# Kernel tuning notes

Measured on AMD Instinct MI355X. Metric: run time of the kernel, lower is better.

## Reference

```python
import jax, jax.numpy as jnp
import numpy as np

B, N, M = 32, 512, 512
EPS = 0.05        # Sinkhorn entropic regularization (approximates exact EMD flow)
N_ITERS = 50      # fixed Sinkhorn iterations
NEG = -1e9        # log(0) surrogate for masked particles


def setup_inputs() -> dict:
    key = jax.random.key(0)
    k1, k2, k3, k4, k5, k6 = jax.random.split(key, 6)
    a_mask = (jax.random.uniform(k1, (B, N)) > 0.1).astype(jnp.float32)
    b_mask = (jax.random.uniform(k2, (B, M)) > 0.1).astype(jnp.float32)
    a_mask = a_mask.at[:, 0].set(1.0)  # guarantee nonempty clouds
    b_mask = b_mask.at[:, 0].set(1.0)
    pc_a = jnp.concatenate([jax.random.normal(k3, (B, N, 2)),
                            jax.random.uniform(k5, (B, N, 1), minval=0.1, maxval=1.0)], axis=-1)
    pc_b = jnp.concatenate([jax.random.normal(k4, (B, M, 2)),
                            jax.random.uniform(k6, (B, M, 1), minval=0.1, maxval=1.0)], axis=-1)
    return {"a_mask": a_mask, "pc_a": pc_a, "b_mask": b_mask, "pc_b": pc_b}


def _sinkhorn_logflow(loga, logb, logK):
    # log-domain Sinkhorn: find P with row sums exp(loga), col sums exp(logb)
    def body(i, carry):
        logu, logv = carry
        logu = loga - jax.scipy.special.logsumexp(logK + logv[:, None, :], axis=2)
        logv = logb - jax.scipy.special.logsumexp(logK + logu[:, :, None], axis=1)
        return (logu, logv)
    logu = jnp.zeros_like(loga)
    logv = jnp.zeros_like(logb)
    logu, logv = jax.lax.fori_loop(0, N_ITERS, body, (logu, logv))
    return logu[:, :, None] + logK + logv[:, None, :]  # [B, N, M]


def _emd_flow(a_pt, b_pt, dist, va, vb):
    # normalized pt distributions (emd(..., norm=True))
    aw = a_pt / jnp.sum(a_pt, axis=-1, keepdims=True)
    bw = b_pt / jnp.sum(b_pt, axis=-1, keepdims=True)
    loga = jnp.where(va, jnp.log(jnp.where(va, aw, 1.0)), NEG)
    logb = jnp.where(vb, jnp.log(jnp.where(vb, bw, 1.0)), NEG)
    logK = -dist / EPS
    flow = jnp.exp(_sinkhorn_logflow(loga, logb, logK))
    return flow * va[:, :, None].astype(flow.dtype) * vb[:, None, :].astype(flow.dtype)


def reference(a_mask, pc_a, b_mask, pc_b):
    a_pt = a_mask * pc_a[..., -1]              # [B, N]
    b_pt = b_mask * pc_b[..., -1]              # [B, M]
    va = a_pt > 0
    vb = b_pt > 0
    # masked pairwise (eta, phi) distance matrix
    diff = pc_a[:, :, None, :2] - pc_b[:, None, :, :2]      # [B, N, M, 2]
    d = jnp.sqrt(jnp.sum(diff * diff, axis=-1) + 1e-12)
    dist = d * va[:, :, None].astype(d.dtype) * vb[:, None, :].astype(d.dtype)
    # optimal-transport flow (detached in the original: computed on CPU numpy)
    flow = jax.lax.stop_gradient(_emd_flow(a_pt, b_pt, dist, va, vb))
    ot_term = jnp.sum(dist * dist * flow, axis=(-1, -2))    # [B]
    # huber_loss(reduction='none'), delta=1
    e = a_pt.sum(axis=-1) - b_pt.sum(axis=-1)
    huber = jnp.where(jnp.abs(e) <= 1.0, 0.5 * e * e, jnp.abs(e) - 0.5)
    return ot_term + huber
```

## Files before the change

kernel.cpp:

```cpp
#include <hip/hip_runtime.h>
#include <math.h>

#define NB 32
#define NP 512
#define RG 8
#define RPB 64
#define ITERS 50
#define EPSV   0.05f
#define INVEPS 20.0f

typedef unsigned long long u64;
typedef unsigned int u32;

#define N_PACK (2*NB*RG*NP)

__device__ __forceinline__ void st32_xchg(u32* p, u32 v) {
  (void)__hip_atomic_exchange(p, v, __ATOMIC_RELAXED, __HIP_MEMORY_SCOPE_AGENT);
}
__device__ __forceinline__ u32 ld32(const u32* p) {
  return __hip_atomic_load(p, __ATOMIC_RELAXED, __HIP_MEMORY_SCOPE_AGENT);
}
__device__ __forceinline__ void st64f(float2* p, float tag, float val) {
  union { float2 f; u64 u; } c; c.f = make_float2(tag, val);
  __hip_atomic_store((u64*)p, c.u, __ATOMIC_RELAXED, __HIP_MEMORY_SCOPE_AGENT);
}
__device__ __forceinline__ float2 ld64f(const float2* p) {
  union { u64 u; float2 f; } c;
  c.u = __hip_atomic_load((const u64*)p, __ATOMIC_RELAXED, __HIP_MEMORY_SCOPE_AGENT);
  return c.f;
}

__device__ __forceinline__ u32 tag_of(int k) {
  return (0x765431u >> (4 * (k % 6))) & 0xFu;
}
__device__ __forceinline__ u32 pack_slot(float v, u32 tag) {
  return (__float_as_uint(v) & ~7u) | tag;
}

__global__ __launch_bounds__(NP) void emd_kernel(
    const float* __restrict__ a_mask, const float* __restrict__ pc_a,
    const float* __restrict__ b_mask, const float* __restrict__ pc_b,
    u32* __restrict__ pack, float2* __restrict__ epi,
    float* __restrict__ out)
{
  const int rb = blockIdx.x;
  const int b  = rb >> 3;
  const int rg = rb & 7;
  const int t  = threadIdx.x;
  const int chunk = t & 7;
  const int lrow  = t >> 3;
  const int grow  = rg*RPB + lrow;
  const int lane  = t & 63, wid = t >> 6;

  __shared__ __align__(16) float rho_l[NP];
  __shared__ __align__(16) float bw_l[NP];
  __shared__ __align__(16) float u_l[RPB];
  __shared__ __align__(16) float sm[NP];
  __shared__ float red[16];

  float4 eKreg[16];
  float  eKcol[RPB];
  float  aw_r, bw_t, hub = 0.f;

  {
    const float apt = a_mask[b*NP+t] * pc_a[((size_t)b*NP+t)*3+2];
    const float bpt = b_mask[b*NP+t] * pc_b[((size_t)b*NP+t)*3+2];
    float ra = apt, rv = bpt;
    #pragma unroll
    for (int o = 32; o; o >>= 1) { ra += __shfl_xor(ra, o); rv += __shfl_xor(rv, o); }
    if (lane == 0) { red[wid] = ra; red[8+wid] = rv; }
    __syncthreads();
    float asum = 0.f, bsum = 0.f;
    #pragma unroll
    for (int w = 0; w < 8; ++w) { asum += red[w]; bsum += red[8+w]; }
    const float e = asum - bsum, ae = fabsf(e);
    hub = (ae <= 1.f) ? 0.5f*e*e : (ae - 0.5f);
    sm[t]   = (apt > 0.f) ? apt/asum : 0.f;
    bw_l[t] = (bpt > 0.f) ? bpt/bsum : 0.f;
    __syncthreads();
    aw_r = sm[grow];
    bw_t = bw_l[t];
    const float ax = pc_a[((size_t)b*NP+grow)*3+0];
    const float ay = pc_a[((size_t)b*NP+grow)*3+1];
    const bool  va = aw_r > 0.f;
    #pragma unroll
    for (int cc = 0; cc < 16; ++cc) {
      float r[4];
      #pragma unroll
      for (int e2 = 0; e2 < 4; ++e2) {
        const int col = 32*cc + 4*chunk + e2;
        const float bx = pc_b[((size_t)b*NP+col)*3+0];
        const float by = pc_b[((size_t)b*NP+col)*3+1];
        const bool  vb = bw_l[col] > 0.f;
        const float dx = ax-bx, dy = ay-by;
        const float d  = sqrtf(dx*dx + dy*dy + 1e-12f);
        r[e2] = (va && vb) ? __expf((-INVEPS)*d) : 1.f;
      }
      eKreg[cc] = make_float4(r[0], r[1], r[2], r[3]);
    }
    const float bx0 = pc_b[((size_t)b*NP+t)*3+0];
    const float by0 = pc_b[((size_t)b*NP+t)*3+1];
    const bool  vb0 = bw_t > 0.f;
    #pragma unroll
    for (int i = 0; i < RPB; ++i) {
      const int row = rg*RPB + i;
      const float axi = pc_a[((size_t)b*NP+row)*3+0];
      const float ayi = pc_a[((size_t)b*NP+row)*3+1];
      const bool  vai = sm[row] > 0.f;
      const float dx = axi-bx0, dy = ayi-by0;
      const float d  = sqrtf(dx*dx + dy*dy + 1e-12f);
      eKcol[i] = (vai && vb0) ? __expf((-INVEPS)*d) : 1.f;
    }
    rho_l[t] = 1.f;
    __syncthreads();
  }

  for (int k = 1; k <= ITERS; ++k) {
    const u32 tag = tag_of(k);
    const int par = k & 1;
    const u32* base = pack + ((size_t)par*NB + b)*RG*NP + t;

    {
      const float4* r4p = (const float4*)rho_l;
      float dot = 0.f;
      #pragma unroll
      for (int cc = 0; cc < 16; ++cc) {
        const float4 g4 = r4p[8*cc + chunk];
        const float4 kk = eKreg[cc];
        dot += kk.x*g4.x + kk.y*g4.y + kk.z*g4.z + kk.w*g4.w;
      }
      #pragma unroll
      for (int o = 4; o; o >>= 1) dot += __shfl_xor(dot, o);
      if (chunk == 0) u_l[lrow] = aw_r / fmaxf(dot, 1e-38f);
    }
    __syncthreads();

    float sc_own;
    {
      const float4* u4p = (const float4*)u_l;
      float sc = 0.f;
      #pragma unroll
      for (int i4 = 0; i4 < 16; ++i4) {
        const float4 uu = u4p[i4];
        sc += eKcol[4*i4+0]*uu.x + eKcol[4*i4+1]*uu.y
            + eKcol[4*i4+2]*uu.z + eKcol[4*i4+3]*uu.w;
      }
      sc_own = sc;
      st32_xchg(pack + (((size_t)par*NB + b)*RG + rg)*NP + t, pack_slot(sc, tag));
    }

    u32 q[RG];
    #pragma unroll
    for (int r = 0; r < RG; ++r)
      if (r != rg) q[r] = ld32(base + (size_t)r*NP);

    {
      unsigned pend = 0xFFu & ~(1u << rg);
      long long sweeps = 0;
      while (true) {
        unsigned np = 0;
        #pragma unroll
        for (int r = 0; r < RG; ++r)
          if ((pend >> r) & 1u)
            if ((q[r] & 7u) != tag) np |= (1u << r);
        pend = np;
        if (!pend) break;
        #pragma unroll
        for (int r = 0; r < RG; ++r)
          if ((pend >> r) & 1u)
            q[r] = ld32(base + (size_t)r*NP);
        if (++sweeps > (1LL<<22)) break;
      }
      float S = sc_own;
      #pragma unroll
      for (int r = 0; r < RG; ++r)
        if (r != rg) S += __uint_as_float(q[r]);
      rho_l[t] = bw_t / fmaxf(S, 1e-38f);
    }
    __syncthreads();
  }

  float acc = 0.f;
  {
    const float ur = u_l[lrow];
    const float4* r4p = (const float4*)rho_l;
    #pragma unroll
    for (int cc = 0; cc < 16; ++cc) {
      const float4 g4 = r4p[8*cc + chunk];
      const float4 kk = eKreg[cc];
      const float ek[4] = {kk.x, kk.y, kk.z, kk.w};
      const float vv[4] = {g4.x, g4.y, g4.z, g4.w};
      #pragma unroll
      for (int e2 = 0; e2 < 4; ++e2) {
        const float lk = __logf(fmaxf(ek[e2], 1e-38f));
        const float d2 = (EPSV*lk)*(EPSV*lk);
        const float v  = d2 * ur * ek[e2] * vv[e2];
        acc += (ek[e2] > 0.f) ? v : 0.f;
      }
    }
  }
  sm[t] = acc;
  __syncthreads();
  if (t < 64) {
    float v = 0.f;
    #pragma unroll
    for (int q2 = 0; q2 < 8; ++q2) v += sm[t*8+q2];
    #pragma unroll
    for (int o = 32; o; o >>= 1) v += __shfl_xor(v, o);
    if (t == 0) st64f(epi + (size_t)b*RG + rg, 51.f, v);
  }
  if (rg == 0 && t < RG) {
    float2 pr;
    long long spins = 0;
    do {
      pr = ld64f(epi + (size_t)b*RG + t);
      if (pr.x == 51.f) break;
      __builtin_amdgcn_s_sleep(1);
    } while (++spins < (1LL<<26));
    float v = pr.y;
    #pragma unroll
    for (int o = 4; o; o >>= 1) v += __shfl_xor(v, o);
    if (t == 0) out[b] = v + hub;
  }
}

extern "C" void kernel_launch(void* const* d_in, const int* in_sizes, int n_in,
                              void* d_out, int out_size, void* d_ws, size_t ws_size,
                              hipStream_t stream) {
  const float* a_mask = (const float*)d_in[0];
  const float* pc_a   = (const float*)d_in[1];
  const float* b_mask = (const float*)d_in[2];
  const float* pc_b   = (const float*)d_in[3];
  float* out = (float*)d_out;
  u32*    pack = (u32*)d_ws;
  float2* epi  = (float2*)(pack + N_PACK);
  (void)in_sizes; (void)n_in; (void)out_size; (void)ws_size;

  emd_kernel<<<NB*RG, NP, 0, stream>>>(a_mask, pc_a, b_mask, pc_b,
                                       pack, epi, out);
}
```

Before: 202.8 us.

## Use four 1024-thread blocks per batch to halve cross-block exchange partners

Each batch is now split across 4 workgroups of 1024 threads instead of 8 of 512, so each block owns 128 rows. The two halves of a block combine their column partial sums through shared memory before publishing them. Each thread then waits on 3 remote slots instead of 7 in the global spin exchange every Sinkhorn iteration. The cost is an extra __syncthreads per iteration, 1024-thread blocks with heavy register use (which may cause spills or lower occupancy), and half the threads idling during the exchange. The atomic exchange is also replaced with a plain atomic store, and the epilogue reduction is simplified.

```diff
diff --git a/kernel.cpp b/kernel.cpp
--- a/kernel.cpp
+++ b/kernel.cpp
@@ -3,8 +3,9 @@
 
 #define NB 32
 #define NP 512
-#define RG 8
-#define RPB 64
+#define RG4 4
+#define RPB4 128
+#define NT 1024
 #define ITERS 50
 #define EPSV   0.05f
 #define INVEPS 20.0f
@@ -12,10 +13,11 @@
 typedef unsigned long long u64;
 typedef unsigned int u32;
 
-#define N_PACK (2*NB*RG*NP)
-
-__device__ __forceinline__ void st32_xchg(u32* p, u32 v) {
-  (void)__hip_atomic_exchange(p, v, __ATOMIC_RELAXED, __HIP_MEMORY_SCOPE_AGENT);
+#define PAR_STRIDE3 (NB*RG4*NP)
+#define N_PACK3 (2*PAR_STRIDE3)
+
+__device__ __forceinline__ void st32(u32* p, u32 v) {
+  __hip_atomic_store(p, v, __ATOMIC_RELAXED, __HIP_MEMORY_SCOPE_AGENT);
 }
 __device__ __forceinline__ u32 ld32(const u32* p) {
   return __hip_atomic_load(p, __ATOMIC_RELAXED, __HIP_MEMORY_SCOPE_AGENT);
@@ -37,49 +39,61 @@
   return (__float_as_uint(v) & ~7u) | tag;
 }
 
-__global__ __launch_bounds__(NP) void emd_kernel(
+__global__ __launch_bounds__(NT) void emd_kernel(
     const float* __restrict__ a_mask, const float* __restrict__ pc_a,
     const float* __restrict__ b_mask, const float* __restrict__ pc_b,
     u32* __restrict__ pack, float2* __restrict__ epi,
     float* __restrict__ out)
 {
   const int rb = blockIdx.x;
-  const int b  = rb >> 3;
-  const int rg = rb & 7;
+  const int b  = rb >> 2;
+  const int g  = rb & 3;
   const int t  = threadIdx.x;
   const int chunk = t & 7;
   const int lrow  = t >> 3;
-  const int grow  = rg*RPB + lrow;
+  const int grow  = g*RPB4 + lrow;
+  const int ct    = t & 511;
+  const int h     = t >> 9;
   const int lane  = t & 63, wid = t >> 6;
 
   __shared__ __align__(16) float rho_l[NP];
   __shared__ __align__(16) float bw_l[NP];
-  __shared__ __align__(16) float u_l[RPB];
+  __shared__ __align__(16) float u_l[RPB4];
   __shared__ __align__(16) float sm[NP];
+  __shared__ __align__(16) float scc[NP];
   __shared__ float red[16];
 
   float4 eKreg[16];
-  float  eKcol[RPB];
+  float  eKcol[64];
   float  aw_r, bw_t, hub = 0.f;
 
+  u32* ownp = pack + ((size_t)(b*RG4 + g))*NP + ct;
+  const u32* base0 = pack + (size_t)b*RG4*NP + ct;
+
   {
-    const float apt = a_mask[b*NP+t] * pc_a[((size_t)b*NP+t)*3+2];
-    const float bpt = b_mask[b*NP+t] * pc_b[((size_t)b*NP+t)*3+2];
-    float ra = apt, rv = bpt;
-    #pragma unroll
-    for (int o = 32; o; o >>= 1) { ra += __shfl_xor(ra, o); rv += __shfl_xor(rv, o); }
-    if (lane == 0) { red[wid] = ra; red[8+wid] = rv; }
+    float apt = 0.f, bpt = 0.f;
+    if (t < NP) {
+      apt = a_mask[b*NP+t] * pc_a[((size_t)b*NP+t)*3+2];
+      bpt = b_mask[b*NP+t] * pc_b[((size_t)b*NP+t)*3+2];
+      float ra = apt, rv = bpt;
+      #pragma unroll
+      for (int o = 32; o; o >>= 1) { ra += __shfl_xor(ra, o); rv += __shfl_xor(rv, o); }
+      if (lane == 0) { red[wid] = ra; red[8+wid] = rv; }
+    }
     __syncthreads();
     float asum = 0.f, bsum = 0.f;
     #pragma unroll
     for (int w = 0; w < 8; ++w) { asum += red[w]; bsum += red[8+w]; }
     const float e = asum - bsum, ae = fabsf(e);
     hub = (ae <= 1.f) ? 0.5f*e*e : (ae - 0.5f);
-    sm[t]   = (apt > 0.f) ? apt/asum : 0.f;
-    bw_l[t] = (bpt > 0.f) ? bpt/bsum : 0.f;
+    if (t < NP) {
+      sm[t]   = (apt > 0.f) ? apt/asum : 0.f;
+      bw_l[t] = (bpt > 0.f) ? bpt/bsum : 0.f;
+      rho_l[t] = 1.f;
+    }
     __syncthreads();
     aw_r = sm[grow];
-    bw_t = bw_l[t];
+    bw_t = bw_l[ct];
     const float ax = pc_a[((size_t)b*NP+grow)*3+0];
     const float ay = pc_a[((size_t)b*NP+grow)*3+1];
     const bool  va = aw_r > 0.f;
@@ -98,12 +112,12 @@
       }
       eKreg[cc] = make_float4(r[0], r[1], r[2], r[3]);
     }
-    const float bx0 = pc_b[((size_t)b*NP+t)*3+0];
-    const float by0 = pc_b[((size_t)b*NP+t)*3+1];
+    const float bx0 = pc_b[((size_t)b*NP+ct)*3+0];
+    const float by0 = pc_b[((size_t)b*NP+ct)*3+1];
     const bool  vb0 = bw_t > 0.f;
     #pragma unroll
-    for (int i = 0; i < RPB; ++i) {
-      const int row = rg*RPB + i;
+    for (int i = 0; i < 64; ++i) {
+      const int row = g*RPB4 + h*64 + i;
       const float axi = pc_a[((size_t)b*NP+row)*3+0];
       const float ayi = pc_a[((size_t)b*NP+row)*3+1];
       const bool  vai = sm[row] > 0.f;
@@ -111,14 +125,12 @@
       const float d  = sqrtf(dx*dx + dy*dy + 1e-12f);
       eKcol[i] = (vai && vb0) ? __expf((-INVEPS)*d) : 1.f;
     }
-    rho_l[t] = 1.f;
     __syncthreads();
   }
 
   for (int k = 1; k <= ITERS; ++k) {
     const u32 tag = tag_of(k);
-    const int par = k & 1;
-    const u32* base = pack + ((size_t)par*NB + b)*RG*NP + t;
+    const size_t po = (size_t)(k & 1) * (size_t)PAR_STRIDE3;
 
     {
       const float4* r4p = (const float4*)rho_l;
@@ -135,47 +147,51 @@
     }
     __syncthreads();
 
-    float sc_own;
+    float sc;
     {
       const float4* u4p = (const float4*)u_l;
-      float sc = 0.f;
+      float s = 0.f;
       #pragma unroll
       for (int i4 = 0; i4 < 16; ++i4) {
-        const float4 uu = u4p[i4];
-        sc += eKcol[4*i4+0]*uu.x + eKcol[4*i4+1]*uu.y
-            + eKcol[4*i4+2]*uu.z + eKcol[4*i4+3]*uu.w;
-      }
-      sc_own = sc;
-      st32_xchg(pack + (((size_t)par*NB + b)*RG + rg)*NP + t, pack_slot(sc, tag));
-    }
-
-    u32 q[RG];
-    #pragma unroll
-    for (int r = 0; r < RG; ++r)
-      if (r != rg) q[r] = ld32(base + (size_t)r*NP);
-
-    {
-      unsigned pend = 0xFFu & ~(1u << rg);
+        const float4 uu = u4p[h*16 + i4];
+        s += eKcol[4*i4+0]*uu.x + eKcol[4*i4+1]*uu.y
+           + eKcol[4*i4+2]*uu.z + eKcol[4*i4+3]*uu.w;
+      }
+      sc = s;
+      if (h == 1) scc[ct] = s;
+    }
+    __syncthreads();
+
+    if (h == 0) {
+      const float stot = sc + scc[ct];
+      st32(ownp + po, pack_slot(stot, tag));
+
+      u32 q[RG4];
+      #pragma unroll
+      for (int r = 0; r < RG4; ++r)
+        if (r != g) q[r] = ld32(base0 + po + (size_t)r*NP);
+
+      unsigned pend = 0xFu & ~(1u << g);
       long long sweeps = 0;
       while (true) {
         unsigned np = 0;
         #pragma unroll
-        for (int r = 0; r < RG; ++r)
+        for (int r = 0; r < RG4; ++r)
           if ((pend >> r) & 1u)
             if ((q[r] & 7u) != tag) np |= (1u << r);
         pend = np;
         if (!pend) break;
         #pragma unroll
-        for (int r = 0; r < RG; ++r)
+        for (int r = 0; r < RG4; ++r)
           if ((pend >> r) & 1u)
-            q[r] = ld32(base + (size_t)r*NP);
+            q[r] = ld32(base0 + po + (size_t)r*NP);
         if (++sweeps > (1LL<<22)) break;
       }
-      float S = sc_own;
-      #pragma unroll
-      for (int r = 0; r < RG; ++r)
-        if (r != rg) S += __uint_as_float(q[r]);
-      rho_l[t] = bw_t / fmaxf(S, 1e-38f);
+      float S = stot;
+      #pragma unroll
+      for (int r = 0; r < RG4; ++r)
+        if (r != g) S += __uint_as_float(q[r]);
+      rho_l[ct] = bw_t / fmaxf(S, 1e-38f);
     }
     __syncthreads();
   }
@@ -199,27 +215,28 @@
       }
     }
   }
-  sm[t] = acc;
+  #pragma unroll
+  for (int o = 32; o; o >>= 1) acc += __shfl_xor(acc, o);
   __syncthreads();
-  if (t < 64) {
+  if (lane == 0) red[wid] = acc;
+  __syncthreads();
+  if (t == 0) {
     float v = 0.f;
     #pragma unroll
-    for (int q2 = 0; q2 < 8; ++q2) v += sm[t*8+q2];
-    #pragma unroll
-    for (int o = 32; o; o >>= 1) v += __shfl_xor(v, o);
-    if (t == 0) st64f(epi + (size_t)b*RG + rg, 51.f, v);
-  }
-  if (rg == 0 && t < RG) {
+    for (int w = 0; w < 16; ++w) v += red[w];
+    st64f(epi + (size_t)b*RG4 + g, 51.f, v);
+  }
+  if (g == 0 && t < RG4) {
     float2 pr;
     long long spins = 0;
     do {
-      pr = ld64f(epi + (size_t)b*RG + t);
+      pr = ld64f(epi + (size_t)b*RG4 + t);
       if (pr.x == 51.f) break;
       __builtin_amdgcn_s_sleep(1);
     } while (++spins < (1LL<<26));
     float v = pr.y;
     #pragma unroll
-    for (int o = 4; o; o >>= 1) v += __shfl_xor(v, o);
+    for (int o = 2; o; o >>= 1) v += __shfl_xor(v, o);
     if (t == 0) out[b] = v + hub;
   }
 }
@@ -233,9 +250,9 @@
   const float* pc_b   = (const float*)d_in[3];
   float* out = (float*)d_out;
   u32*    pack = (u32*)d_ws;
-  float2* epi  = (float2*)(pack + N_PACK);
+  float2* epi  = (float2*)(pack + N_PACK3);
   (void)in_sizes; (void)n_in; (void)out_size; (void)ws_size;
 
-  emd_kernel<<<NB*RG, NP, 0, stream>>>(a_mask, pc_a, b_mask, pc_b,
-                                       pack, epi, out);
-}
+  emd_kernel<<<NB*RG4, NT, 0, stream>>>(a_mask, pc_a, b_mask, pc_b,
+                                        pack, epi, out);
+}
```

After: 324.2 us. 1.6x slower.
